# Kernel tuning notes

Measured on AMD Instinct MI355X. Metric: run time of the kernel, lower is better.

## Reference

```python
import jax, jax.numpy as jnp
import numpy as np

N, E, D_IN, D_OUT, H = 50000, 800000, 128, 128, 4
D_H = D_OUT // H


def setup_inputs() -> dict:
    key = jax.random.key(0)
    ks = jax.random.split(key, 6)
    x = jax.random.normal(ks[0], (N, D_IN), dtype=jnp.float32)
    edge_index = jax.random.randint(ks[1], (2, E), 0, N, dtype=jnp.int64)
    # parameters (xavier-ish scaling)
    W = jax.random.normal(ks[2], (D_IN, D_OUT), dtype=jnp.float32) * (1.0 / np.sqrt(D_IN))
    attn_vec = jax.random.normal(ks[3], (H, 2 * D_H), dtype=jnp.float32) * (1.0 / np.sqrt(2 * D_H))
    out_w = jax.random.normal(ks[4], (D_OUT, D_OUT), dtype=jnp.float32) * (1.0 / np.sqrt(D_OUT))
    out_b = jax.random.normal(ks[5], (D_OUT,), dtype=jnp.float32) * 0.01
    return {"x": x, "edge_index": edge_index, "W": W, "attn_vec": attn_vec,
            "out_w": out_w, "out_b": out_b}


def reference(x, edge_index, W, attn_vec, out_w, out_b):
    n = x.shape[0]
    Wx = (x @ W).reshape(n, H, D_H)                      # [N,H,d_h]
    src, dst = edge_index[0], edge_index[1]
    h_src = Wx[src]                                      # [E,H,d_h]
    h_dst = Wx[dst]                                      # [E,H,d_h]
    a_i = attn_vec[:, :D_H]                              # [H,d_h]
    a_j = attn_vec[:, D_H:]                              # [H,d_h]
    e = jnp.einsum('ehd,hd->eh', h_src, a_i) + jnp.einsum('ehd,hd->eh', h_dst, a_j)
    e = jax.nn.leaky_relu(e, negative_slope=0.2)         # [E,H]
    # segment softmax over incoming edges per destination node
    e_max = jax.ops.segment_max(e, dst, num_segments=n)  # [N,H]
    exp_e = jnp.exp(e - e_max[dst])                      # [E,H]
    exp_sum = jax.ops.segment_sum(exp_e, dst, num_segments=n)  # [N,H]
    alpha = exp_e / (exp_sum[dst] + 1e-16)               # [E,H]
    # weighted scatter-add aggregation
    agg = jax.ops.segment_sum(alpha[:, :, None] * h_src, dst, num_segments=n)  # [N,H,d_h]
    out = agg.reshape(n, D_OUT) @ out_w + out_b
    return jax.nn.elu(out)
```

## Files before the change

### kernel.cpp

```cpp
#include <hip/hip_runtime.h>
#include <math.h>


typedef __attribute__((ext_vector_type(8))) short short8;
typedef __attribute__((ext_vector_type(4))) float f32x4;

#define BIN_VPT 16

__device__ __forceinline__ float lrelu(float v) { return v >= 0.f ? v : 0.2f * v; }

__device__ __forceinline__ unsigned short f2bf(float f) {
  unsigned int u = __float_as_uint(f);
  u += 0x7FFFu + ((u >> 16) & 1u);
  return (unsigned short)(u >> 16);
}
__device__ __forceinline__ unsigned int cvt_pk_bf16(float lo, float hi) {
  unsigned int r;
  asm("v_cvt_pk_bf16_f32 %0, %1, %2" : "=v"(r) : "v"(lo), "v"(hi));
  return r;
}
__device__ __forceinline__ float bflo(unsigned int w) { return __uint_as_float(w << 16); }
__device__ __forceinline__ float bfhi(unsigned int w) { return __uint_as_float(w & 0xFFFF0000u); }

__device__ __forceinline__ int blk_excl_scan(int v, int* ws) {
  const int t = threadIdx.x, lane = t & 63, wv = t >> 6;
  int incl = v;
#pragma unroll
  for (int m = 1; m < 64; m <<= 1) {
    int x = __shfl_up(incl, m, 64);
    if (lane >= m) incl += x;
  }
  if (lane == 63) ws[wv] = incl;
  __syncthreads();
  int woff = 0;
  for (int p = 0; p < wv; ++p) woff += ws[p];
  return woff + incl - v;
}

__global__ void k_setup(const float* __restrict__ W, const float* __restrict__ ow,
                        unsigned short* __restrict__ wf, unsigned short* __restrict__ owf,
                        int* __restrict__ gcnt, int* __restrict__ gcur) {
  const int t = blockIdx.x * 256 + threadIdx.x;
  if (blockIdx.x == 0) gcnt[threadIdx.x] = 0;
  if (blockIdx.x == 1) gcur[threadIdx.x] = 0;
  const int which = t >> 11;
  const int tt = t & 2047;
  const float* M = which ? ow : W;
  unsigned short* F = which ? owf : wf;
  const int lane = tt & 63;
  const int nt = (tt >> 6) & 7;
  const int ks = tt >> 9;
  const int k0 = ks * 32 + (lane >> 4) * 8;
  const int col = nt * 16 + (lane & 15);
  short8 v;
#pragma unroll
  for (int j = 0; j < 8; ++j) v[j] = (short)f2bf(M[(k0 + j) * 128 + col]);
  *(short8*)(F + (size_t)tt * 8) = v;
}

__global__ void k_gemm1b(const float* __restrict__ x, const unsigned short* __restrict__ wf,
                         const float* __restrict__ attn, unsigned int* __restrict__ Wxb,
                         float* __restrict__ s_i, float* __restrict__ s_j, int n,
                         const int* __restrict__ dst, int* __restrict__ gcnt, int E,
                         int gemmBlocks) {
  __shared__ int lc[256];
  if (blockIdx.x >= gemmBlocks) {
    const int bb = blockIdx.x - gemmBlocks;
    lc[threadIdx.x] = 0;
    __syncthreads();
    const int base = bb * (256 * BIN_VPT);
#pragma unroll
    for (int j = 0; j < BIN_VPT; ++j) {
      int e = base + j * 256 + threadIdx.x;
      if (e < E) atomicAdd(&lc[((unsigned int)dst[e]) >> 8], 1);
    }
    __syncthreads();
    int c = lc[threadIdx.x];
    if (c) atomicAdd(&gcnt[threadIdx.x], c);
    return;
  }

  const int lane = threadIdx.x & 63;
  const int gw = blockIdx.x * (blockDim.x >> 6) + (threadIdx.x >> 6);
  const int r0 = gw * 16;
  if (r0 >= n) return;
  const int g = lane >> 4, c = lane & 15;

  f32x4 acc[8];
#pragma unroll
  for (int nt = 0; nt < 8; ++nt) acc[nt] = (f32x4){0.f, 0.f, 0.f, 0.f};

  const int arow = min(r0 + c, n - 1);
#pragma unroll
  for (int ks = 0; ks < 4; ++ks) {
    const float* xr = x + (size_t)arow * 128 + ks * 32 + g * 8;
    float4 v0 = *(const float4*)xr;
    float4 v1 = *(const float4*)(xr + 4);
    uint4 au;
    au.x = cvt_pk_bf16(v0.x, v0.y);
    au.y = cvt_pk_bf16(v0.z, v0.w);
    au.z = cvt_pk_bf16(v1.x, v1.y);
    au.w = cvt_pk_bf16(v1.z, v1.w);
    short8 af = __builtin_bit_cast(short8, au);
#pragma unroll
    for (int nt = 0; nt < 8; ++nt) {
      short8 bf = *(const short8*)(wf + ((size_t)(ks * 8 + nt) * 64 + lane) * 8);
      acc[nt] = __builtin_amdgcn_mfma_f32_16x16x32_bf16(af, bf, acc[nt], 0, 0, 0);
    }
  }

  const int odd = c & 1;
#pragma unroll
  for (int r = 0; r < 4; ++r) {
    const int row = r0 + g * 4 + r;
    if (row >= n) continue;
    unsigned int* dp = Wxb + (size_t)row * 64;
#pragma unroll
    for (int ntp = 0; ntp < 4; ++ntp) {
      float ve = acc[ntp][r], vo = acc[ntp + 4][r];
      float vex = __shfl_xor(ve, 1, 64);
      float vox = __shfl_xor(vo, 1, 64);
      const int nt = odd ? ntp + 4 : ntp;
      dp[nt * 8 + (c >> 1)] = cvt_pk_bf16(odd ? vox : ve, odd ? vo : vex);
    }
  }

  float aiv[8], ajv[8];
#pragma unroll
  for (int nt = 0; nt < 8; ++nt) {
    const int hh = nt >> 1, ch = (nt & 1) * 16 + c;
    aiv[nt] = attn[hh * 64 + ch];
    ajv[nt] = attn[hh * 64 + 32 + ch];
  }
#pragma unroll
  for (int r = 0; r < 4; ++r) {
    float pih[4], pjh[4];
#pragma unroll
    for (int h = 0; h < 4; ++h) {
      pih[h] = acc[2 * h][r] * aiv[2 * h] + acc[2 * h + 1][r] * aiv[2 * h + 1];
      pjh[h] = acc[2 * h][r] * ajv[2 * h] + acc[2 * h + 1][r] * ajv[2 * h + 1];
    }
#pragma unroll
    for (int m = 1; m < 16; m <<= 1) {
#pragma unroll
      for (int h = 0; h < 4; ++h) {
        pih[h] += __shfl_xor(pih[h], m, 64);
        pjh[h] += __shfl_xor(pjh[h], m, 64);
      }
    }
    const int row = r0 + g * 4 + r;
    if (c == 0 && row < n) {
#pragma unroll
      for (int h = 0; h < 4; ++h) {
        s_i[(size_t)row * 4 + h] = pih[h];
        s_j[(size_t)row * 4 + h] = pjh[h];
      }
    }
  }
}

__global__ void k_bin1(const int* __restrict__ edges, const int* __restrict__ gcnt,
                       int* __restrict__ gcur, unsigned int* __restrict__ tmp, int E) {
  __shared__ int ws[4];
  __shared__ int bst_s[256];
  __shared__ int lcnt[256];
  __shared__ int lbase[256];
  const int t = threadIdx.x;
  const int excl = blk_excl_scan(gcnt[t], ws);
  bst_s[t] = excl;
  lcnt[t] = 0;
  __syncthreads();
  const int base = blockIdx.x * (256 * BIN_VPT);
  unsigned int pv[BIN_VPT];
  int rk[BIN_VPT];
#pragma unroll
  for (int j = 0; j < BIN_VPT; ++j) {
    int e = base + j * 256 + t;
    if (e < E) {
      unsigned int s = (unsigned int)edges[e];
      unsigned int d = (unsigned int)edges[E + e];
      pv[j] = s | (d << 16);
      rk[j] = atomicAdd(&lcnt[d >> 8], 1);
    } else {
      pv[j] = 0u;
      rk[j] = -1;
    }
  }
  __syncthreads();
  const int c = lcnt[t];
  lbase[t] = bst_s[t] + (c ? atomicAdd(&gcur[t], c) : 0);
  __syncthreads();
#pragma unroll
  for (int j = 0; j < BIN_VPT; ++j) {
    if (rk[j] >= 0) {
      const int b = pv[j] >> 24;
      tmp[lbase[b] + rk[j]] = pv[j];
    }
  }
}

__global__ void k_bin2(const unsigned int* __restrict__ tmp, const int* __restrict__ gcnt,
                       int* __restrict__ csr, int* __restrict__ offs,
                       int* __restrict__ cnts, int n) {
  __shared__ int ws[4];
  __shared__ int bst_s[256];
  __shared__ int nc[256];
  const int b = blockIdx.x;
  const int t = threadIdx.x;
  bst_s[t] = blk_excl_scan(gcnt[t], ws);
  nc[t] = 0;
  __syncthreads();
  const int base = bst_s[b], cnt = gcnt[b];
  for (int i = t; i < cnt; i += 256)
    atomicAdd(&nc[(tmp[base + i] >> 16) & 255], 1);
  __syncthreads();
  const int node = b * 256 + t;
  const int c = nc[t];
  if (node < n) cnts[node] = c;
  __syncthreads();
  const int excl = blk_excl_scan(c, ws);
  if (node < n) offs[node] = base + excl;
  __syncthreads();
  nc[t] = excl;
  __syncthreads();
  for (int i = t; i < cnt; i += 256) {
    unsigned int v = tmp[base + i];
    int pos = atomicAdd(&nc[(v >> 16) & 255], 1);
    csr[base + pos] = (int)(v & 0xFFFFu);
  }
}

#define AGG_PAIR(e)                                                       \
  {                                                                       \
    const int eA_ = (e) + half;                                           \
    const int s_ = lsrc[wv][eA_];                                         \
    const float p_ = lp[wv][eA_][hq];                                     \
    uint2 w_ = *(const uint2*)(WxbL + ((size_t)s_ << 6));                 \
    a0 += p_ * bflo(w_.x); a1 += p_ * bfhi(w_.x);                         \
    a2 += p_ * bflo(w_.y); a3 += p_ * bfhi(w_.y);                         \
    smh += p_;                                                            \
  }
#define AGG_SINGLE(e)                                                     \
  {                                                                       \
    const int s_ = lsrc[wv][e];                                           \
    const float p_ = half ? 0.f : lp[wv][e][hq];                          \
    uint2 w_ = *(const uint2*)(WxbL + ((size_t)s_ << 6));                 \
    a0 += p_ * bflo(w_.x); a1 += p_ * bfhi(w_.x);                         \
    a2 += p_ * bflo(w_.y); a3 += p_ * bfhi(w_.y);                         \
    smh += p_;                                                            \
  }

__global__ void k_aggm(const unsigned int* __restrict__ Wxb, const float* __restrict__ s_i,
                       const float* __restrict__ s_j, const int* __restrict__ offs,
                       const int* __restrict__ cnts, const int* __restrict__ csr_src,
                       const unsigned short* __restrict__ owf, const float* __restrict__ ob,
                       float* __restrict__ out, int n) {
  __shared__ unsigned int aTile[16][65];
  __shared__ int   lsrc[4][64];
  __shared__ float lp[4][64][4];
  const int lane = threadIdx.x & 63;
  const int wv = threadIdx.x >> 6;
  const int nd0 = blockIdx.x * 16;
  const int nd0w = nd0 + wv * 4;
  const int h = lane >> 4;
  const int half = lane >> 5;
  const int cq = lane & 31;
  const int hq = cq >> 3;
  const unsigned int* WxbL = Wxb + (cq << 1);

  int degv = 0;
  if (lane < 4 && nd0w + lane < n) degv = cnts[nd0w + lane];
  const int wbase = (nd0w < n) ? offs[nd0w] : 0;
  const int d0 = __shfl(degv, 0, 64), d1 = __shfl(degv, 1, 64);
  const int d2 = __shfl(degv, 2, 64), d3 = __shfl(degv, 3, 64);
  const int tot = d0 + d1 + d2 + d3;

  int cur = 0;
  int rem = d0;
  float a0 = 0.f, a1 = 0.f, a2 = 0.f, a3 = 0.f;
  float smh = 0.f;

  while (cur < 4 && rem == 0) {
    if (nd0w + cur < n) aTile[(wv << 2) + cur][lane] = 0u;
    ++cur;
    rem = (cur == 1) ? d1 : (cur == 2) ? d2 : (cur == 3) ? d3 : 0;
  }

  for (int c0 = 0; c0 < tot; c0 += 64) {
    const int m = min(64, tot - c0);
    if (lane < m) {
      const int src = csr_src[wbase + c0 + lane];
      const int pos = c0 + lane;
      const int nl = (pos >= d0) + (pos >= d0 + d1) + (pos >= d0 + d1 + d2);
      const float4 sj = *(const float4*)(s_j + (size_t)(nd0w + nl) * 4);
      const float4 si = *(const float4*)(s_i + (size_t)src * 4);
      float4 p;
      p.x = __expf(lrelu(si.x + sj.x));
      p.y = __expf(lrelu(si.y + sj.y));
      p.z = __expf(lrelu(si.z + sj.z));
      p.w = __expf(lrelu(si.w + sj.w));
      lsrc[wv][lane] = src;
      *(float4*)&lp[wv][lane][0] = p;
    }
    asm volatile("s_waitcnt lgkmcnt(0)" ::: "memory");
    int k = 0;
    while (k < m) {
      const int take = min(m - k, rem);
      const int npair2 = take & ~1;
      int e = k;
      const int endp = k + npair2;
      for (; e + 8 <= endp; e += 8) {
        AGG_PAIR(e) AGG_PAIR(e + 2) AGG_PAIR(e + 4) AGG_PAIR(e + 6)
      }
      for (; e < endp; e += 2) AGG_PAIR(e)
      if (take & 1) AGG_SINGLE(k + npair2)
      k += take;
      rem -= take;
      while (rem == 0 && cur < 4) {
        float f0 = a0 + __shfl_xor(a0, 32, 64);
        float f1 = a1 + __shfl_xor(a1, 32, 64);
        float f2 = a2 + __shfl_xor(a2, 32, 64);
        float f3 = a3 + __shfl_xor(a3, 32, 64);
        float st = smh + __shfl_xor(smh, 32, 64);
        const float inv = 1.f / (st + 1e-16f);
        if (half == 0 && nd0w + cur < n) {
          aTile[(wv << 2) + cur][(cq << 1) + 0] = cvt_pk_bf16(f0 * inv, f1 * inv);
          aTile[(wv << 2) + cur][(cq << 1) + 1] = cvt_pk_bf16(f2 * inv, f3 * inv);
        }
        ++cur;
        a0 = a1 = a2 = a3 = 0.f; smh = 0.f;
        rem = (cur == 1) ? d1 : (cur == 2) ? d2 : (cur == 3) ? d3 : 0;
      }
      if (cur >= 4) break;
    }
  }
  __syncthreads();

  const int g = lane >> 4, c = lane & 15;
#pragma unroll
  for (int t2 = 0; t2 < 2; ++t2) {
    const int nt = wv + t2 * 4;
    f32x4 o = (f32x4){0.f, 0.f, 0.f, 0.f};
#pragma unroll
    for (int ks = 0; ks < 4; ++ks) {
      uint4 au = *(const uint4*)&aTile[c][ks * 16 + g * 4];
      short8 af = __builtin_bit_cast(short8, au);
      short8 bf = *(const short8*)(owf + ((size_t)(ks * 8 + nt) * 64 + lane) * 8);
      o = __builtin_amdgcn_mfma_f32_16x16x32_bf16(af, bf, o, 0, 0, 0);
    }
#pragma unroll
    for (int r = 0; r < 4; ++r) {
      const int row = nd0 + g * 4 + r;
      if (row < n) {
        float v = o[r] + ob[nt * 16 + c];
        v = v > 0.f ? v : expm1f(v);
        out[(size_t)row * 128 + nt * 16 + c] = v;
      }
    }
  }
}

extern "C" void kernel_launch(void* const* d_in, const int* in_sizes, int n_in,
                              void* d_out, int out_size, void* d_ws, size_t ws_size,
                              hipStream_t stream) {
  const float* x    = (const float*)d_in[0];
  const int*   edges = (const int*)d_in[1];
  const float* W    = (const float*)d_in[2];
  const float* attn = (const float*)d_in[3];
  const float* ow   = (const float*)d_in[4];
  const float* ob   = (const float*)d_in[5];
  const int n = in_sizes[0] / 128;
  const int E = in_sizes[1] / 2;
  float* out = (float*)d_out;

  char* wp = (char*)d_ws;
  auto alloc = [&](size_t bytes) {
    char* p = wp;
    wp += (bytes + 255) & ~(size_t)255;
    return p;
  };
  unsigned short* wf  = (unsigned short*)alloc(2048 * 8 * 2);
  unsigned short* owf = (unsigned short*)alloc(2048 * 8 * 2);
  unsigned int*   Wxb = (unsigned int*)alloc((size_t)n * 64 * 4);
  float* s_i    = (float*)alloc((size_t)n * 4 * 4);
  float* s_j    = (float*)alloc((size_t)n * 4 * 4);
  int*   gcnt   = (int*)alloc(256 * 4);
  int*   gcur   = (int*)alloc(256 * 4);
  int*   offs   = (int*)alloc((size_t)n * 4);
  int*   cnts   = (int*)alloc((size_t)n * 4);
  unsigned int* tmp = (unsigned int*)alloc((size_t)E * 4);
  int*   csr    = (int*)alloc((size_t)E * 4);

  dim3 blk(256);
  const int NB = (n + 255) / 256;
  const int EB = (E + 256 * BIN_VPT - 1) / (256 * BIN_VPT);
  const int strips = (n + 15) / 16;
  const int gemmBlocks = (strips + 3) / 4;

  k_setup<<<16, blk, 0, stream>>>(W, ow, wf, owf, gcnt, gcur);
  k_gemm1b<<<gemmBlocks + EB, blk, 0, stream>>>(x, wf, attn, Wxb, s_i, s_j, n,
                                                edges + E, gcnt, E, gemmBlocks);
  k_bin1<<<EB, blk, 0, stream>>>(edges, gcnt, gcur, tmp, E);
  k_bin2<<<NB, blk, 0, stream>>>(tmp, gcnt, csr, offs, cnts, n);
  k_aggm<<<(n + 15) / 16, blk, 0, stream>>>(Wxb, s_i, s_j, offs, cnts, csr,
                                            owf, ob, out, n);
}
```

Measured before the change: 97.16 us.

## Pad per-node CSR segments to multiples of four and aggregate with 16B gathers

Pads each destination node's CSR edge list to a multiple of four with sentinel entries, which are masked out by zeroing their attention weight. With that padding, the aggregation kernel has 16 lanes per edge, each loading 16 bytes (8 bf16 features), and processes four edges in parallel per wave. Before, 32 lanes per edge each loaded 8 bytes. This widens the gather loads and removes the odd-edge tail path, at the cost of extra padded work, a two-step cross-lane reduction, and larger scratch buffers.

```diff
diff --git a/kernel.cpp b/kernel.cpp
--- a/kernel.cpp
+++ b/kernel.cpp
@@ -6,6 +6,7 @@
 typedef __attribute__((ext_vector_type(4))) float f32x4;
 
 #define BIN_VPT 16
+#define BKT_PAD 768
 
 __device__ __forceinline__ float lrelu(float v) { return v >= 0.f ? v : 0.2f * v; }
 
@@ -166,7 +167,7 @@
   __shared__ int lcnt[256];
   __shared__ int lbase[256];
   const int t = threadIdx.x;
-  const int excl = blk_excl_scan(gcnt[t], ws);
+  const int excl = blk_excl_scan(gcnt[t] + BKT_PAD, ws);
   bst_s[t] = excl;
   lcnt[t] = 0;
   __syncthreads();
@@ -207,7 +208,7 @@
   __shared__ int nc[256];
   const int b = blockIdx.x;
   const int t = threadIdx.x;
-  bst_s[t] = blk_excl_scan(gcnt[t], ws);
+  bst_s[t] = blk_excl_scan(gcnt[t] + BKT_PAD, ws);
   nc[t] = 0;
   __syncthreads();
   const int base = bst_s[b], cnt = gcnt[b];
@@ -216,9 +217,10 @@
   __syncthreads();
   const int node = b * 256 + t;
   const int c = nc[t];
-  if (node < n) cnts[node] = c;
-  __syncthreads();
-  const int excl = blk_excl_scan(c, ws);
+  const int pc = (c + 3) & ~3;
+  if (node < n) cnts[node] = pc;
+  __syncthreads();
+  const int excl = blk_excl_scan(pc, ws);
   if (node < n) offs[node] = base + excl;
   __syncthreads();
   nc[t] = excl;
@@ -228,25 +230,19 @@
     int pos = atomicAdd(&nc[(v >> 16) & 255], 1);
     csr[base + pos] = (int)(v & 0xFFFFu);
   }
-}
-
-#define AGG_PAIR(e)                                                       \
+  for (int i = c; i < pc; ++i) csr[base + excl + i] = (int)0x80000000u;
+}
+
+#define AGG_STEP(e)                                                       \
   {                                                                       \
-    const int eA_ = (e) + half;                                           \
+    const int eA_ = (e) + g;                                              \
     const int s_ = lsrc[wv][eA_];                                         \
     const float p_ = lp[wv][eA_][hq];                                     \
-    uint2 w_ = *(const uint2*)(WxbL + ((size_t)s_ << 6));                 \
+    uint4 w_ = *(const uint4*)(WxbL + ((size_t)s_ << 6));                 \
     a0 += p_ * bflo(w_.x); a1 += p_ * bfhi(w_.x);                         \
     a2 += p_ * bflo(w_.y); a3 += p_ * bfhi(w_.y);                         \
-    smh += p_;                                                            \
-  }
-#define AGG_SINGLE(e)                                                     \
-  {                                                                       \
-    const int s_ = lsrc[wv][e];                                           \
-    const float p_ = half ? 0.f : lp[wv][e][hq];                          \
-    uint2 w_ = *(const uint2*)(WxbL + ((size_t)s_ << 6));                 \
-    a0 += p_ * bflo(w_.x); a1 += p_ * bfhi(w_.x);                         \
-    a2 += p_ * bflo(w_.y); a3 += p_ * bfhi(w_.y);                         \
+    a4 += p_ * bflo(w_.z); a5 += p_ * bfhi(w_.z);                         \
+    a6 += p_ * bflo(w_.w); a7 += p_ * bfhi(w_.w);                         \
     smh += p_;                                                            \
   }
 
@@ -255,18 +251,17 @@
                        const int* __restrict__ cnts, const int* __restrict__ csr_src,
                        const unsigned short* __restrict__ owf, const float* __restrict__ ob,
                        float* __restrict__ out, int n) {
-  __shared__ unsigned int aTile[16][65];
+  __shared__ unsigned int aTile[16][68];
   __shared__ int   lsrc[4][64];
   __shared__ float lp[4][64][4];
   const int lane = threadIdx.x & 63;
   const int wv = threadIdx.x >> 6;
   const int nd0 = blockIdx.x * 16;
   const int nd0w = nd0 + wv * 4;
-  const int h = lane >> 4;
-  const int half = lane >> 5;
-  const int cq = lane & 31;
-  const int hq = cq >> 3;
-  const unsigned int* WxbL = Wxb + (cq << 1);
+  const int g = lane >> 4;
+  const int cl = lane & 15;
+  const int hq = cl >> 2;
+  const unsigned int* WxbL = Wxb + (cl << 2);
 
   int degv = 0;
   if (lane < 4 && nd0w + lane < n) degv = cnts[nd0w + lane];
@@ -278,6 +273,7 @@
   int cur = 0;
   int rem = d0;
   float a0 = 0.f, a1 = 0.f, a2 = 0.f, a3 = 0.f;
+  float a4 = 0.f, a5 = 0.f, a6 = 0.f, a7 = 0.f;
   float smh = 0.f;
 
   while (cur < 4 && rem == 0) {
@@ -289,16 +285,18 @@
   for (int c0 = 0; c0 < tot; c0 += 64) {
     const int m = min(64, tot - c0);
     if (lane < m) {
-      const int src = csr_src[wbase + c0 + lane];
+      const unsigned int sv = (unsigned int)csr_src[wbase + c0 + lane];
+      const int src = (int)(sv & 0xFFFFu);
+      const float live = (sv >> 31) ? 0.f : 1.f;
       const int pos = c0 + lane;
       const int nl = (pos >= d0) + (pos >= d0 + d1) + (pos >= d0 + d1 + d2);
       const float4 sj = *(const float4*)(s_j + (size_t)(nd0w + nl) * 4);
       const float4 si = *(const float4*)(s_i + (size_t)src * 4);
       float4 p;
-      p.x = __expf(lrelu(si.x + sj.x));
-      p.y = __expf(lrelu(si.y + sj.y));
-      p.z = __expf(lrelu(si.z + sj.z));
-      p.w = __expf(lrelu(si.w + sj.w));
+      p.x = live * __expf(lrelu(si.x + sj.x));
+      p.y = live * __expf(lrelu(si.y + sj.y));
+      p.z = live * __expf(lrelu(si.z + sj.z));
+      p.w = live * __expf(lrelu(si.w + sj.w));
       lsrc[wv][lane] = src;
       *(float4*)&lp[wv][lane][0] = p;
     }
@@ -306,29 +304,36 @@
     int k = 0;
     while (k < m) {
       const int take = min(m - k, rem);
-      const int npair2 = take & ~1;
       int e = k;
-      const int endp = k + npair2;
-      for (; e + 8 <= endp; e += 8) {
-        AGG_PAIR(e) AGG_PAIR(e + 2) AGG_PAIR(e + 4) AGG_PAIR(e + 6)
+      const int end = k + take;
+      for (; e + 16 <= end; e += 16) {
+        AGG_STEP(e) AGG_STEP(e + 4) AGG_STEP(e + 8) AGG_STEP(e + 12)
       }
-      for (; e < endp; e += 2) AGG_PAIR(e)
-      if (take & 1) AGG_SINGLE(k + npair2)
+      for (; e < end; e += 4) AGG_STEP(e)
       k += take;
       rem -= take;
       while (rem == 0 && cur < 4) {
-        float f0 = a0 + __shfl_xor(a0, 32, 64);
-        float f1 = a1 + __shfl_xor(a1, 32, 64);
-        float f2 = a2 + __shfl_xor(a2, 32, 64);
-        float f3 = a3 + __shfl_xor(a3, 32, 64);
-        float st = smh + __shfl_xor(smh, 32, 64);
+        float f0 = a0, f1 = a1, f2 = a2, f3 = a3;
+        float f4 = a4, f5 = a5, f6 = a6, f7 = a7, st = smh;
+#pragma unroll
+        for (int mm = 16; mm < 64; mm <<= 1) {
+          f0 += __shfl_xor(f0, mm, 64); f1 += __shfl_xor(f1, mm, 64);
+          f2 += __shfl_xor(f2, mm, 64); f3 += __shfl_xor(f3, mm, 64);
+          f4 += __shfl_xor(f4, mm, 64); f5 += __shfl_xor(f5, mm, 64);
+          f6 += __shfl_xor(f6, mm, 64); f7 += __shfl_xor(f7, mm, 64);
+          st += __shfl_xor(st, mm, 64);
+        }
         const float inv = 1.f / (st + 1e-16f);
-        if (half == 0 && nd0w + cur < n) {
-          aTile[(wv << 2) + cur][(cq << 1) + 0] = cvt_pk_bf16(f0 * inv, f1 * inv);
-          aTile[(wv << 2) + cur][(cq << 1) + 1] = cvt_pk_bf16(f2 * inv, f3 * inv);
+        if (g == 0 && nd0w + cur < n) {
+          uint4 pk;
+          pk.x = cvt_pk_bf16(f0 * inv, f1 * inv);
+          pk.y = cvt_pk_bf16(f2 * inv, f3 * inv);
+          pk.z = cvt_pk_bf16(f4 * inv, f5 * inv);
+          pk.w = cvt_pk_bf16(f6 * inv, f7 * inv);
+          *(uint4*)&aTile[(wv << 2) + cur][cl << 2] = pk;
         }
         ++cur;
-        a0 = a1 = a2 = a3 = 0.f; smh = 0.f;
+        a0 = a1 = a2 = a3 = a4 = a5 = a6 = a7 = 0.f; smh = 0.f;
         rem = (cur == 1) ? d1 : (cur == 2) ? d2 : (cur == 3) ? d3 : 0;
       }
       if (cur >= 4) break;
@@ -336,21 +341,21 @@
   }
   __syncthreads();
 
-  const int g = lane >> 4, c = lane & 15;
+  const int g2 = lane >> 4, c = lane & 15;
 #pragma unroll
   for (int t2 = 0; t2 < 2; ++t2) {
     const int nt = wv + t2 * 4;
     f32x4 o = (f32x4){0.f, 0.f, 0.f, 0.f};
 #pragma unroll
     for (int ks = 0; ks < 4; ++ks) {
-      uint4 au = *(const uint4*)&aTile[c][ks * 16 + g * 4];
+      uint4 au = *(const uint4*)&aTile[c][ks * 16 + g2 * 4];
       short8 af = __builtin_bit_cast(short8, au);
       short8 bf = *(const short8*)(owf + ((size_t)(ks * 8 + nt) * 64 + lane) * 8);
       o = __builtin_amdgcn_mfma_f32_16x16x32_bf16(af, bf, o, 0, 0, 0);
     }
 #pragma unroll
     for (int r = 0; r < 4; ++r) {
-      const int row = nd0 + g * 4 + r;
+      const int row = nd0 + g2 * 4 + r;
       if (row < n) {
         float v = o[r] + ob[nt * 16 + c];
         v = v > 0.f ? v : expm1f(v);
@@ -388,8 +393,9 @@
   int*   gcur   = (int*)alloc(256 * 4);
   int*   offs   = (int*)alloc((size_t)n * 4);
   int*   cnts   = (int*)alloc((size_t)n * 4);
-  unsigned int* tmp = (unsigned int*)alloc((size_t)E * 4);
-  int*   csr    = (int*)alloc((size_t)E * 4);
+  const size_t padded = (size_t)E + 256 * BKT_PAD;
+  unsigned int* tmp = (unsigned int*)alloc(padded * 4);
+  int*   csr    = (int*)alloc(padded * 4);
 
   dim3 blk(256);
   const int NB = (n + 255) / 256;
```

Result: slower. 100.9 us (+3.9%).
